# Optimization experiments

Hardware: AMD Instinct MI355X
Metric: run time of the kernel (lower is better)

## Reference

```python
import jax, jax.numpy as jnp
import numpy as np
from jax import lax

B, T = 2048, 256
V, E, H = 128, 128, 64
POS_WEIGHT = 20.0


def setup_inputs() -> dict:
    key = jax.random.key(0)
    ks = jax.random.split(key, 9)
    # indices in [1, V) so padding_idx=0 row (zeroed) is unused
    x = jax.random.randint(ks[0], (B, T), 1, V)
    targets = (jax.random.uniform(ks[1], (B,)) < 0.05).astype(jnp.float32)
    emb = jax.random.normal(ks[2], (V, E), dtype=jnp.float32).at[0].set(0.0)  # padding_idx=0
    k = 1.0 / np.sqrt(H)
    W_ih = jax.random.uniform(ks[3], (4 * H, E), minval=-k, maxval=k, dtype=jnp.float32)
    W_hh = jax.random.uniform(ks[4], (4 * H, H), minval=-k, maxval=k, dtype=jnp.float32)
    b_ih = jax.random.uniform(ks[5], (4 * H,), minval=-k, maxval=k, dtype=jnp.float32)
    b_hh = jax.random.uniform(ks[6], (4 * H,), minval=-k, maxval=k, dtype=jnp.float32)
    W_fc = jax.random.uniform(ks[7], (1, H), minval=-k, maxval=k, dtype=jnp.float32)
    b_fc = jax.random.uniform(ks[8], (1,), minval=-k, maxval=k, dtype=jnp.float32)
    return {"x": x, "targets": targets, "emb": emb, "W_ih": W_ih, "W_hh": W_hh,
            "b_ih": b_ih, "b_hh": b_hh, "W_fc": W_fc, "b_fc": b_fc}


def reference(x, targets, emb, W_ih, W_hh, b_ih, b_hh, W_fc, b_fc):
    xe = emb[x]  # [B, T, E]
    # precompute input-to-hidden projections for all timesteps: [B, T, 4H]
    xp = jnp.einsum('bte,ge->btg', xe, W_ih) + b_ih + b_hh
    h0 = jnp.zeros((xe.shape[0], W_hh.shape[1]), dtype=xe.dtype)
    c0 = jnp.zeros_like(h0)

    def step(carry, xt):
        h, c = carry
        gates = xt + h @ W_hh.T  # [B, 4H], PyTorch gate order: i, f, g, o
        i, f, g, o = jnp.split(gates, 4, axis=-1)
        c = jax.nn.sigmoid(f) * c + jax.nn.sigmoid(i) * jnp.tanh(g)
        h = jax.nn.sigmoid(o) * jnp.tanh(c)
        return (h, c), None

    (hT, _), _ = lax.scan(step, (h0, c0), jnp.swapaxes(xp, 0, 1))  # scan over time
    logits = (hT @ W_fc.T + b_fc)[:, 0]  # [B]
    # BCEWithLogits with pos_weight, mean reduction (numerically stable)
    loss = -(POS_WEIGHT * targets * jax.nn.log_sigmoid(logits)
             + (1.0 - targets) * jax.nn.log_sigmoid(-logits)).mean()
    return logits, loss
```

## Files before the change

### kernel.cpp

```cpp
#include <hip/hip_runtime.h>
#include <stdint.h>

#define B_ 2048
#define T_ 256
#define V_ 128
#define E_ 128
#define H_ 64
#define G4_ 256
#define POS_W 20.0f
#define MB_ 4
#define NBLK_ (B_ / MB_)
typedef _Float16 half1;
typedef __attribute__((ext_vector_type(8))) _Float16 f16x8;
typedef __attribute__((ext_vector_type(4))) float f32x4;

#if __has_builtin(__builtin_amdgcn_exp2f)
#define EXP2F(x) __builtin_amdgcn_exp2f(x)
#else
#define EXP2F(x) exp2f(x)
#endif

#if __has_builtin(__builtin_amdgcn_rcpf)
#define RCPF(x) __builtin_amdgcn_rcpf(x)
#else
#define RCPF(x) (1.0f / (x))
#endif

__device__ __forceinline__ float sigm(float x) {
    return RCPF(1.0f + EXP2F(-1.44269504f * x));
}
__device__ __forceinline__ float tanhr(float x) {
    float t = EXP2F(2.88539008f * x);
    return 1.0f - 2.0f * RCPF(t + 1.0f);
}

__device__ __forceinline__ void lds_barrier() {
    asm volatile("s_waitcnt lgkmcnt(0)\n\ts_barrier" ::: "memory");
}

__global__ void k_prep(const float* __restrict__ emb, const float* __restrict__ Wih,
                       const float* __restrict__ bih, const float* __restrict__ bhh,
                       float* __restrict__ projC, float* __restrict__ loss_slot) {
    int tid = threadIdx.x;
    int v = blockIdx.x;
    if (v == 0 && tid == 0) *loss_slot = 0.0f;
    int u = tid >> 2, g = tid & 3;
    int row = g * 64 + u;
    const float4* e4 = (const float4*)(emb + v * E_);
    const float4* w4 = (const float4*)(Wih + row * E_);
    float acc = bih[row] + bhh[row];
#pragma unroll
    for (int i = 0; i < E_ / 4; ++i) {
        float4 a = e4[i];
        float4 b = w4[i];
        acc += a.x * b.x + a.y * b.y + a.z * b.z + a.w * b.w;
    }
    projC[v * G4_ + tid] = acc;
}

__launch_bounds__(256, 2)
__global__ void k_lstm(const int* __restrict__ x, const float* __restrict__ Whh,
                       const float* __restrict__ projC, const float* __restrict__ Wfc,
                       const float* __restrict__ bfc, const float* __restrict__ targets,
                       float* __restrict__ logits, float* __restrict__ loss_slot) {
    int b0 = blockIdx.x * MB_;
    int t = threadIdx.x;
    int w = t >> 6, l = t & 63;
    int q = l >> 4, cc = l & 15;
    int u = 16 * w + cc;

    __shared__ __align__(16) half1 hf[2][1024];
    __shared__ int xT[T_][MB_];
    __shared__ float hfin[MB_][68];
    __shared__ float zred[MB_];

#pragma unroll
    for (int i = 0; i < MB_; ++i) xT[t][i] = x[(b0 + i) * T_ + t];
    ((float*)hf)[t] = 0.0f;
    ((float*)hf)[t + 256] = 0.0f;
    ((float*)hf)[t + 512] = 0.0f;
    ((float*)hf)[t + 768] = 0.0f;
    __syncthreads();

    f16x8 bf[4][2];
#pragma unroll
    for (int jj = 0; jj < 4; ++jj) {
#pragma unroll
        for (int c = 0; c < 2; ++c) {
            int row = jj * 64 + 16 * w + cc;
            int kb = c * 32 + q * 8;
            float4 w0 = *(const float4*)(Whh + row * H_ + kb);
            float4 w1 = *(const float4*)(Whh + row * H_ + kb + 4);
            f16x8 tmp;
            tmp[0] = (half1)w0.x; tmp[1] = (half1)w0.y;
            tmp[2] = (half1)w0.z; tmp[3] = (half1)w0.w;
            tmp[4] = (half1)w1.x; tmp[5] = (half1)w1.y;
            tmp[6] = (half1)w1.z; tmp[7] = (half1)w1.w;
            bf[jj][c] = tmp;
        }
    }

    int hbase = (u >> 5) * 512 + ((u >> 3) & 3) * 128 + (4 * q) * 8 + (u & 7);

    float cA = 0.0f, hA = 0.0f;

    f32x4 ppA = *(const f32x4*)(projC + xT[0][q] * G4_ + u * 4);
    f32x4 pnA = *(const f32x4*)(projC + xT[1][q] * G4_ + u * 4);

    int p = 0;
#pragma unroll 2
    for (int step = 0; step < T_; ++step) {
        f32x4 p2A = *(const f32x4*)(projC + xT[(step + 2) & (T_ - 1)][q] * G4_ + u * 4);

        const f16x8 a0 = *(const f16x8*)(hf[p] + l * 8);
        const f16x8 a1 = *(const f16x8*)(hf[p] + 512 + l * 8);

        f32x4 z4 = {0.0f, 0.0f, 0.0f, 0.0f};
        float gA[4];
#pragma unroll
        for (int jj = 0; jj < 4; ++jj) {
            f32x4 d0 = __builtin_amdgcn_mfma_f32_16x16x32_f16(a0, bf[jj][0], z4, 0, 0, 0);
            f32x4 d1 = __builtin_amdgcn_mfma_f32_16x16x32_f16(a1, bf[jj][1], z4, 0, 0, 0);
            gA[jj] = d0[0] + d1[0];
        }

        float iA = sigm(gA[0] + ppA.x);
        float fA = sigm(gA[1] + ppA.y);
        float ggA = tanhr(gA[2] + ppA.z);
        float oA = sigm(gA[3] + ppA.w);
        cA = fA * cA + iA * ggA;
        hA = oA * tanhr(cA);

        hf[p ^ 1][hbase] = (half1)hA;

        ppA = pnA;
        pnA = p2A;
        p ^= 1;
        lds_barrier();
    }

    hfin[q][u] = hA;
    __syncthreads();
    int m4 = t >> 6, uu = t & 63;
    float part = hfin[m4][uu] * Wfc[uu];
#pragma unroll
    for (int off = 32; off > 0; off >>= 1) part += __shfl_down(part, off, 64);
    if (uu == 0) {
        float z = part + bfc[0];
        logits[b0 + m4] = z;
        float tg = targets[b0 + m4];
        float e = EXP2F(-1.44269504f * fabsf(z));
        float lsp = fminf(z, 0.0f) - log1pf(e);
        float lsn = lsp - z;
        zred[m4] = -(POS_W * tg * lsp + (1.0f - tg) * lsn) * (1.0f / (float)B_);
    }
    __syncthreads();
    if (t == 0) {
        float s = 0.0f;
#pragma unroll
        for (int i = 0; i < MB_; ++i) s += zred[i];
        atomicAdd(loss_slot, s);
    }
}

extern "C" void kernel_launch(void* const* d_in, const int* in_sizes, int n_in,
                              void* d_out, int out_size, void* d_ws, size_t ws_size,
                              hipStream_t stream) {
    const int* x = (const int*)d_in[0];
    const float* targets = (const float*)d_in[1];
    const float* emb = (const float*)d_in[2];
    const float* Wih = (const float*)d_in[3];
    const float* Whh = (const float*)d_in[4];
    const float* bih = (const float*)d_in[5];
    const float* bhh = (const float*)d_in[6];
    const float* Wfc = (const float*)d_in[7];
    const float* bfc = (const float*)d_in[8];
    float* out = (float*)d_out;

    float* projC = (float*)d_ws;

    k_prep<<<dim3(V_), dim3(256), 0, stream>>>(emb, Wih, bih, bhh, projC, out + B_);
    k_lstm<<<dim3(NBLK_), dim3(256), 0, stream>>>(x, Whh, projC, Wfc, bfc, targets, out,
                                                  out + B_);
}
```

Before: 163.5 us.

## Give each wavefront its own batch row to drop per-step block barriers

Each wavefront now handles one batch row and all 64 hidden units. Before, four waves shared four rows with a block-wide barrier every timestep. The full W_hh now lives in registers per wave (32 f16x8 fragments), and the recurrent state is replicated four times in a private LDS buffer. That makes the recurrence wave-local, so the s_barrier in the time loop goes away. The cost is 4x the MFMA work per step, with most of each result thrown away, plus much higher register pressure that may limit occupancy. It also depends on in-wave LDS ordering with no explicit wait or double buffering.

```diff
diff --git a/kernel.cpp b/kernel.cpp
--- a/kernel.cpp
+++ b/kernel.cpp
@@ -8,8 +8,8 @@
 #define H_ 64
 #define G4_ 256
 #define POS_W 20.0f
-#define MB_ 4
-#define NBLK_ (B_ / MB_)
+#define CH_ 544
+
 typedef _Float16 half1;
 typedef __attribute__((ext_vector_type(8))) _Float16 f16x8;
 typedef __attribute__((ext_vector_type(4))) float f32x4;
@@ -32,10 +32,6 @@
 __device__ __forceinline__ float tanhr(float x) {
     float t = EXP2F(2.88539008f * x);
     return 1.0f - 2.0f * RCPF(t + 1.0f);
-}
-
-__device__ __forceinline__ void lds_barrier() {
-    asm volatile("s_waitcnt lgkmcnt(0)\n\ts_barrier" ::: "memory");
 }
 
 __global__ void k_prep(const float* __restrict__ emb, const float* __restrict__ Wih,
@@ -63,104 +59,109 @@
                        const float* __restrict__ projC, const float* __restrict__ Wfc,
                        const float* __restrict__ bfc, const float* __restrict__ targets,
                        float* __restrict__ logits, float* __restrict__ loss_slot) {
-    int b0 = blockIdx.x * MB_;
     int t = threadIdx.x;
     int w = t >> 6, l = t & 63;
     int q = l >> 4, cc = l & 15;
-    int u = 16 * w + cc;
+    int row = blockIdx.x * 4 + w;
 
-    __shared__ __align__(16) half1 hf[2][1024];
-    __shared__ int xT[T_][MB_];
-    __shared__ float hfin[MB_][68];
-    __shared__ float zred[MB_];
+    __shared__ __align__(16) half1 hf[4][2 * CH_];
+    __shared__ __align__(16) int tok[4][T_];
+    __shared__ float zred[4];
 
+    {
+        int4 tk = *(const int4*)(x + row * T_ + 4 * l);
+        *(int4*)&tok[w][4 * l] = tk;
+    }
+    {
+        uint32_t* hz = (uint32_t*)hf[w];
 #pragma unroll
-    for (int i = 0; i < MB_; ++i) xT[t][i] = x[(b0 + i) * T_ + t];
-    ((float*)hf)[t] = 0.0f;
-    ((float*)hf)[t + 256] = 0.0f;
-    ((float*)hf)[t + 512] = 0.0f;
-    ((float*)hf)[t + 768] = 0.0f;
-    __syncthreads();
+        for (int i = 0; i < 8; ++i) hz[l + 64 * i] = 0u;
+        if (l < 32) hz[512 + l] = 0u;
+    }
 
-    f16x8 bf[4][2];
+    f16x8 bf[16][2];
 #pragma unroll
-    for (int jj = 0; jj < 4; ++jj) {
+    for (int g = 0; g < 4; ++g) {
 #pragma unroll
-        for (int c = 0; c < 2; ++c) {
-            int row = jj * 64 + 16 * w + cc;
-            int kb = c * 32 + q * 8;
-            float4 w0 = *(const float4*)(Whh + row * H_ + kb);
-            float4 w1 = *(const float4*)(Whh + row * H_ + kb + 4);
-            f16x8 tmp;
-            tmp[0] = (half1)w0.x; tmp[1] = (half1)w0.y;
-            tmp[2] = (half1)w0.z; tmp[3] = (half1)w0.w;
-            tmp[4] = (half1)w1.x; tmp[5] = (half1)w1.y;
-            tmp[6] = (half1)w1.z; tmp[7] = (half1)w1.w;
-            bf[jj][c] = tmp;
+        for (int uq = 0; uq < 4; ++uq) {
+            int r = g * 64 + 16 * uq + cc;
+#pragma unroll
+            for (int c = 0; c < 2; ++c) {
+                int kb = c * 32 + q * 8;
+                float4 w0 = *(const float4*)(Whh + r * H_ + kb);
+                float4 w1 = *(const float4*)(Whh + r * H_ + kb + 4);
+                f16x8 tmp;
+                tmp[0] = (half1)w0.x; tmp[1] = (half1)w0.y;
+                tmp[2] = (half1)w0.z; tmp[3] = (half1)w0.w;
+                tmp[4] = (half1)w1.x; tmp[5] = (half1)w1.y;
+                tmp[6] = (half1)w1.z; tmp[7] = (half1)w1.w;
+                bf[g * 4 + uq][c] = tmp;
+            }
         }
     }
 
-    int hbase = (u >> 5) * 512 + ((u >> 3) & 3) * 128 + (4 * q) * 8 + (u & 7);
+    int wbase = (l >> 5) * CH_ + ((l & 31) >> 3) * 128 + (l & 7);
 
-    float cA = 0.0f, hA = 0.0f;
+    float cS = 0.0f, hS = 0.0f;
 
-    f32x4 ppA = *(const f32x4*)(projC + xT[0][q] * G4_ + u * 4);
-    f32x4 pnA = *(const f32x4*)(projC + xT[1][q] * G4_ + u * 4);
+    f32x4 pp = *(const f32x4*)(projC + tok[w][0] * G4_ + 4 * l);
+    f32x4 pn = *(const f32x4*)(projC + tok[w][1] * G4_ + 4 * l);
 
-    int p = 0;
-#pragma unroll 2
     for (int step = 0; step < T_; ++step) {
-        f32x4 p2A = *(const f32x4*)(projC + xT[(step + 2) & (T_ - 1)][q] * G4_ + u * 4);
+        int tk2 = tok[w][(step + 2) & (T_ - 1)];
+        f32x4 p2 = *(const f32x4*)(projC + tk2 * G4_ + 4 * l);
 
-        const f16x8 a0 = *(const f16x8*)(hf[p] + l * 8);
-        const f16x8 a1 = *(const f16x8*)(hf[p] + 512 + l * 8);
+        f16x8 a0 = *(const f16x8*)&hf[w][l * 8];
+        f16x8 a1 = *(const f16x8*)&hf[w][CH_ + l * 8];
 
         f32x4 z4 = {0.0f, 0.0f, 0.0f, 0.0f};
-        float gA[4];
+        float gv[4];
 #pragma unroll
-        for (int jj = 0; jj < 4; ++jj) {
-            f32x4 d0 = __builtin_amdgcn_mfma_f32_16x16x32_f16(a0, bf[jj][0], z4, 0, 0, 0);
-            f32x4 d1 = __builtin_amdgcn_mfma_f32_16x16x32_f16(a1, bf[jj][1], z4, 0, 0, 0);
-            gA[jj] = d0[0] + d1[0];
+        for (int g = 0; g < 4; ++g) {
+            f32x4 dA = __builtin_amdgcn_mfma_f32_16x16x32_f16(a0, bf[g * 4 + 0][0], z4, 0, 0, 0);
+            dA = __builtin_amdgcn_mfma_f32_16x16x32_f16(a1, bf[g * 4 + 0][1], dA, 0, 0, 0);
+            f32x4 dB = __builtin_amdgcn_mfma_f32_16x16x32_f16(a0, bf[g * 4 + 1][0], z4, 0, 0, 0);
+            dB = __builtin_amdgcn_mfma_f32_16x16x32_f16(a1, bf[g * 4 + 1][1], dB, 0, 0, 0);
+            f32x4 dC = __builtin_amdgcn_mfma_f32_16x16x32_f16(a0, bf[g * 4 + 2][0], z4, 0, 0, 0);
+            dC = __builtin_amdgcn_mfma_f32_16x16x32_f16(a1, bf[g * 4 + 2][1], dC, 0, 0, 0);
+            f32x4 dD = __builtin_amdgcn_mfma_f32_16x16x32_f16(a0, bf[g * 4 + 3][0], z4, 0, 0, 0);
+            dD = __builtin_amdgcn_mfma_f32_16x16x32_f16(a1, bf[g * 4 + 3][1], dD, 0, 0, 0);
+            float lo = (q == 0) ? dA[0] : dB[0];
+            float hi = (q == 2) ? dC[0] : dD[0];
+            gv[g] = (q < 2) ? lo : hi;
         }
 
-        float iA = sigm(gA[0] + ppA.x);
-        float fA = sigm(gA[1] + ppA.y);
-        float ggA = tanhr(gA[2] + ppA.z);
-        float oA = sigm(gA[3] + ppA.w);
-        cA = fA * cA + iA * ggA;
-        hA = oA * tanhr(cA);
+        float i_ = sigm(gv[0] + pp.x);
+        float f_ = sigm(gv[1] + pp.y);
+        float g_ = tanhr(gv[2] + pp.z);
+        float o_ = sigm(gv[3] + pp.w);
+        cS = f_ * cS + i_ * g_;
+        hS = o_ * tanhr(cS);
 
-        hf[p ^ 1][hbase] = (half1)hA;
+        half1 hv = (half1)hS;
+        hf[w][wbase] = hv;
+        hf[w][wbase + 32] = hv;
+        hf[w][wbase + 64] = hv;
+        hf[w][wbase + 96] = hv;
 
-        ppA = pnA;
-        pnA = p2A;
-        p ^= 1;
-        lds_barrier();
+        pp = pn;
+        pn = p2;
     }
 
-    hfin[q][u] = hA;
-    __syncthreads();
-    int m4 = t >> 6, uu = t & 63;
-    float part = hfin[m4][uu] * Wfc[uu];
+    float part = hS * Wfc[l];
 #pragma unroll
     for (int off = 32; off > 0; off >>= 1) part += __shfl_down(part, off, 64);
-    if (uu == 0) {
+    if (l == 0) {
         float z = part + bfc[0];
-        logits[b0 + m4] = z;
-        float tg = targets[b0 + m4];
+        logits[row] = z;
+        float tg = targets[row];
         float e = EXP2F(-1.44269504f * fabsf(z));
         float lsp = fminf(z, 0.0f) - log1pf(e);
         float lsn = lsp - z;
-        zred[m4] = -(POS_W * tg * lsp + (1.0f - tg) * lsn) * (1.0f / (float)B_);
+        zred[w] = -(POS_W * tg * lsp + (1.0f - tg) * lsn) * (1.0f / (float)B_);
     }
     __syncthreads();
-    if (t == 0) {
-        float s = 0.0f;
-#pragma unroll
-        for (int i = 0; i < MB_; ++i) s += zred[i];
-        atomicAdd(loss_slot, s);
-    }
+    if (t == 0) atomicAdd(loss_slot, zred[0] + zred[1] + zred[2] + zred[3]);
 }
 
 extern "C" void kernel_launch(void* const* d_in, const int* in_sizes, int n_in,
@@ -180,6 +181,6 @@
     float* projC = (float*)d_ws;
 
     k_prep<<<dim3(V_), dim3(256), 0, stream>>>(emb, Wih, bih, bhh, projC, out + B_);
-    k_lstm<<<dim3(NBLK_), dim3(256), 0, stream>>>(x, Whh, projC, Wfc, bfc, targets, out,
-                                                  out + B_);
+    k_lstm<<<dim3(B_ / 4), dim3(256), 0, stream>>>(x, Whh, projC, Wfc, bfc, targets, out,
+                                                   out + B_);
 }
```

New measurement: 249.3 us. +52.5%, slower.

## Ping-pong two batch groups per block to overlap MFMA and nonlinearity phases

Applied to the files above, without the earlier changes.

Each block now holds two independent 4-sequence groups (512 threads). The groups run offset by half a step, so one group issues its matrix products while the other computes the gate activations, with two barriers per step. The aim is to overlap MFMA latency with transcendental ALU work across waves. It doubles the number of barriers per step and couples the two groups, and the launch bounds change from two blocks of 256 to one block of 512 per CU.

```diff
diff --git a/kernel.cpp b/kernel.cpp
--- a/kernel.cpp
+++ b/kernel.cpp
@@ -8,8 +8,7 @@
 #define H_ 64
 #define G4_ 256
 #define POS_W 20.0f
-#define MB_ 4
-#define NBLK_ (B_ / MB_)
+
 typedef _Float16 half1;
 typedef __attribute__((ext_vector_type(8))) _Float16 f16x8;
 typedef __attribute__((ext_vector_type(4))) float f32x4;
@@ -58,28 +57,33 @@
     projC[v * G4_ + tid] = acc;
 }
 
-__launch_bounds__(256, 2)
+__launch_bounds__(512, 1)
 __global__ void k_lstm(const int* __restrict__ x, const float* __restrict__ Whh,
                        const float* __restrict__ projC, const float* __restrict__ Wfc,
                        const float* __restrict__ bfc, const float* __restrict__ targets,
                        float* __restrict__ logits, float* __restrict__ loss_slot) {
-    int b0 = blockIdx.x * MB_;
+    int b0 = blockIdx.x * 8;
     int t = threadIdx.x;
-    int w = t >> 6, l = t & 63;
+    int w8 = t >> 6, l = t & 63;
+    int grp = t >> 8;
+    int wl = w8 & 3;
+    int tg = t & 255;
     int q = l >> 4, cc = l & 15;
-    int u = 16 * w + cc;
-
-    __shared__ __align__(16) half1 hf[2][1024];
-    __shared__ int xT[T_][MB_];
-    __shared__ float hfin[MB_][68];
-    __shared__ float zred[MB_];
-
-#pragma unroll
-    for (int i = 0; i < MB_; ++i) xT[t][i] = x[(b0 + i) * T_ + t];
+    int u = 16 * wl + cc;
+    int bg = b0 + 4 * grp;
+    bool isY = (grp == 1);
+
+    __shared__ __align__(16) half1 hf[2][2][1024];
+    __shared__ int xT[2][T_][4];
+    __shared__ float hfin[2][4][68];
+    __shared__ float zred[8];
+
+#pragma unroll
+    for (int i = 0; i < 4; ++i) xT[grp][tg][i] = x[(bg + i) * T_ + tg];
     ((float*)hf)[t] = 0.0f;
-    ((float*)hf)[t + 256] = 0.0f;
     ((float*)hf)[t + 512] = 0.0f;
-    ((float*)hf)[t + 768] = 0.0f;
+    ((float*)hf)[t + 1024] = 0.0f;
+    ((float*)hf)[t + 1536] = 0.0f;
     __syncthreads();
 
     f16x8 bf[4][2];
@@ -87,7 +91,7 @@
     for (int jj = 0; jj < 4; ++jj) {
 #pragma unroll
         for (int c = 0; c < 2; ++c) {
-            int row = jj * 64 + 16 * w + cc;
+            int row = jj * 64 + 16 * wl + cc;
             int kb = c * 32 + q * 8;
             float4 w0 = *(const float4*)(Whh + row * H_ + kb);
             float4 w1 = *(const float4*)(Whh + row * H_ + kb + 4);
@@ -103,62 +107,79 @@
     int hbase = (u >> 5) * 512 + ((u >> 3) & 3) * 128 + (4 * q) * 8 + (u & 7);
 
     float cA = 0.0f, hA = 0.0f;
-
-    f32x4 ppA = *(const f32x4*)(projC + xT[0][q] * G4_ + u * 4);
-    f32x4 pnA = *(const f32x4*)(projC + xT[1][q] * G4_ + u * 4);
-
+    float gA[4];
+
+    f32x4 pp = *(const f32x4*)(projC + xT[grp][0][q] * G4_ + u * 4);
+    f32x4 pn = *(const f32x4*)(projC + xT[grp][1][q] * G4_ + u * 4);
     int p = 0;
-#pragma unroll 2
+
+#define PHASE_MFMA()                                                                     \
+    {                                                                                    \
+        const f16x8 a0 = *(const f16x8*)&hf[grp][p][l * 8];                              \
+        const f16x8 a1 = *(const f16x8*)&hf[grp][p][512 + l * 8];                        \
+        f32x4 z4 = {0.0f, 0.0f, 0.0f, 0.0f};                                             \
+        _Pragma("unroll") for (int jj = 0; jj < 4; ++jj) {                               \
+            f32x4 d0 = __builtin_amdgcn_mfma_f32_16x16x32_f16(a0, bf[jj][0], z4, 0, 0, 0); \
+            f32x4 d1 = __builtin_amdgcn_mfma_f32_16x16x32_f16(a1, bf[jj][1], z4, 0, 0, 0); \
+            gA[jj] = d0[0] + d1[0];                                                      \
+        }                                                                                \
+    }
+
+#define PHASE_NONLIN(tstep)                                                              \
+    {                                                                                    \
+        f32x4 p2 = *(const f32x4*)(projC + xT[grp][((tstep) + 2) & (T_ - 1)][q] * G4_ +  \
+                                   u * 4);                                               \
+        float i_ = sigm(gA[0] + pp.x);                                                   \
+        float f_ = sigm(gA[1] + pp.y);                                                   \
+        float g_ = tanhr(gA[2] + pp.z);                                                  \
+        float o_ = sigm(gA[3] + pp.w);                                                   \
+        cA = f_ * cA + i_ * g_;                                                          \
+        hA = o_ * tanhr(cA);                                                             \
+        hf[grp][p ^ 1][hbase] = (half1)hA;                                               \
+        pp = pn;                                                                         \
+        pn = p2;                                                                         \
+        p ^= 1;                                                                          \
+    }
+
     for (int step = 0; step < T_; ++step) {
-        f32x4 p2A = *(const f32x4*)(projC + xT[(step + 2) & (T_ - 1)][q] * G4_ + u * 4);
-
-        const f16x8 a0 = *(const f16x8*)(hf[p] + l * 8);
-        const f16x8 a1 = *(const f16x8*)(hf[p] + 512 + l * 8);
-
-        f32x4 z4 = {0.0f, 0.0f, 0.0f, 0.0f};
-        float gA[4];
-#pragma unroll
-        for (int jj = 0; jj < 4; ++jj) {
-            f32x4 d0 = __builtin_amdgcn_mfma_f32_16x16x32_f16(a0, bf[jj][0], z4, 0, 0, 0);
-            f32x4 d1 = __builtin_amdgcn_mfma_f32_16x16x32_f16(a1, bf[jj][1], z4, 0, 0, 0);
-            gA[jj] = d0[0] + d1[0];
+        if (!isY) {
+            PHASE_MFMA();
+        } else if (step > 0) {
+            PHASE_NONLIN(step - 1);
         }
-
-        float iA = sigm(gA[0] + ppA.x);
-        float fA = sigm(gA[1] + ppA.y);
-        float ggA = tanhr(gA[2] + ppA.z);
-        float oA = sigm(gA[3] + ppA.w);
-        cA = fA * cA + iA * ggA;
-        hA = oA * tanhr(cA);
-
-        hf[p ^ 1][hbase] = (half1)hA;
-
-        ppA = pnA;
-        pnA = p2A;
-        p ^= 1;
         lds_barrier();
-    }
-
-    hfin[q][u] = hA;
+        if (!isY) {
+            PHASE_NONLIN(step);
+        } else {
+            PHASE_MFMA();
+        }
+        lds_barrier();
+    }
+    if (isY) {
+        PHASE_NONLIN(T_ - 1);
+    }
+
+    hfin[grp][q][u] = hA;
     __syncthreads();
-    int m4 = t >> 6, uu = t & 63;
-    float part = hfin[m4][uu] * Wfc[uu];
+    int rr = w8 & 3;
+    int rowg = b0 + 4 * (w8 >> 2) + rr;
+    float part = hfin[w8 >> 2][rr][l] * Wfc[l];
 #pragma unroll
     for (int off = 32; off > 0; off >>= 1) part += __shfl_down(part, off, 64);
-    if (uu == 0) {
+    if (l == 0) {
         float z = part + bfc[0];
-        logits[b0 + m4] = z;
-        float tg = targets[b0 + m4];
+        logits[rowg] = z;
+        float tgt = targets[rowg];
         float e = EXP2F(-1.44269504f * fabsf(z));
         float lsp = fminf(z, 0.0f) - log1pf(e);
         float lsn = lsp - z;
-        zred[m4] = -(POS_W * tg * lsp + (1.0f - tg) * lsn) * (1.0f / (float)B_);
+        zred[w8] = -(POS_W * tgt * lsp + (1.0f - tgt) * lsn) * (1.0f / (float)B_);
     }
     __syncthreads();
     if (t == 0) {
         float s = 0.0f;
 #pragma unroll
-        for (int i = 0; i < MB_; ++i) s += zred[i];
+        for (int i = 0; i < 8; ++i) s += zred[i];
         atomicAdd(loss_slot, s);
     }
 }
@@ -180,6 +201,6 @@
     float* projC = (float*)d_ws;
 
     k_prep<<<dim3(V_), dim3(256), 0, stream>>>(emb, Wih, bih, bhh, projC, out + B_);
-    k_lstm<<<dim3(NBLK_), dim3(256), 0, stream>>>(x, Whh, projC, Wfc, bfc, targets, out,
-                                                  out + B_);
-}
+    k_lstm<<<dim3(B_ / 8), dim3(512), 0, stream>>>(x, Whh, projC, Wfc, bfc, targets, out,
+                                                   out + B_);
+}
```

New measurement: 196.9 us. 1.2x slower.
